# Optimization experiments

Measured on AMD Instinct MI355X. Metric: run time of the kernel, lower is better.

## Reference

```python
import jax, jax.numpy as jnp
import numpy as np

N = 16384


def setup_inputs() -> dict:
    key = jax.random.key(0)
    k1, k2 = jax.random.split(key)
    logits = jax.random.normal(k1, (N,), dtype=jnp.float32)
    targets = jax.random.randint(k2, (N,), 0, 2, dtype=jnp.int64)
    return {"logits": logits, "targets": targets}


def reference(logits, targets):
    # sigmoid scores for every sample
    s = jax.nn.sigmoid(logits)  # [N]
    pos = (targets != 0).astype(s.dtype)  # [N] mask of positives
    neg = (targets == 0).astype(s.dtype)  # [N] mask of negatives
    # all-pairs pos-vs-neg surrogate: (1 - (s_pos - s_neg))^2
    d = 1.0 - (s[:, None] - s[None, :])  # [N, N]
    loss = jnp.sum((pos[:, None] * neg[None, :]) * (d * d))
    n_pos = jnp.sum(pos)
    n_neg = jnp.sum(neg)
    return loss / (n_pos * n_neg)
```

## Files before the change

### kernel.cpp

```cpp
#include <hip/hip_runtime.h>


#define G1 64
#define B1 64

__global__ __launch_bounds__(B1) void auc_partial_kernel(
    const float* __restrict__ logits, const int* __restrict__ targets,
    float* __restrict__ ws, int n) {
  const int gtid = blockIdx.x * B1 + threadIdx.x;
  const int nthreads = G1 * B1;

  float acc[6] = {0.f, 0.f, 0.f, 0.f, 0.f, 0.f};

  const int n4 = n >> 2;
  const float4* l4 = reinterpret_cast<const float4*>(logits);
  const int4*   t4 = reinterpret_cast<const int4*>(targets);

  for (int i = gtid; i < n4; i += nthreads) {
    float4 lv = l4[i];
    int4   tv = t4[i];
    float xs[4] = {lv.x, lv.y, lv.z, lv.w};
    int   ts[4] = {tv.x, tv.y, tv.z, tv.w};
#pragma unroll
    for (int k = 0; k < 4; ++k) {
      float s  = 1.0f / (1.0f + __expf(-xs[k]));
      float s2 = s * s;
      float p  = (ts[k] != 0) ? 1.0f : 0.0f;
      float q  = 1.0f - p;
      acc[0] += p;       acc[1] += q;
      acc[2] += p * s;   acc[3] += q * s;
      acc[4] += p * s2;  acc[5] += q * s2;
    }
  }
  for (int i = (n4 << 2) + gtid; i < n; i += nthreads) {
    float s  = 1.0f / (1.0f + __expf(-logits[i]));
    float s2 = s * s;
    float p  = (targets[i] != 0) ? 1.0f : 0.0f;
    float q  = 1.0f - p;
    acc[0] += p;       acc[1] += q;
    acc[2] += p * s;   acc[3] += q * s;
    acc[4] += p * s2;  acc[5] += q * s2;
  }

#pragma unroll
  for (int j = 0; j < 6; ++j) {
#pragma unroll
    for (int m = 1; m < 64; m <<= 1) {
      acc[j] += __shfl_xor(acc[j], m, 64);
    }
  }

  if (threadIdx.x == 0) {
#pragma unroll
    for (int j = 0; j < 6; ++j) ws[blockIdx.x * 6 + j] = acc[j];
  }
}

__global__ __launch_bounds__(64) void auc_combine_kernel(
    const float* __restrict__ ws, float* __restrict__ out) {
  const int lane = threadIdx.x;

  double t[6];
#pragma unroll
  for (int j = 0; j < 6; ++j) t[j] = (double)ws[lane * 6 + j];

#pragma unroll
  for (int j = 0; j < 6; ++j) {
#pragma unroll
    for (int m = 1; m < 64; m <<= 1) {
      t[j] += __shfl_xor(t[j], m, 64);
    }
  }

  if (lane == 0) {
    double np_ = t[0], nn = t[1], sp = t[2], sn = t[3], sp2 = t[4], sn2 = t[5];
    double loss = np_ * nn
                - 2.0 * nn * sp
                + 2.0 * np_ * sn
                + nn * sp2
                + np_ * sn2
                - 2.0 * sp * sn;
    out[0] = (float)(loss / (np_ * nn));
  }
}

extern "C" void kernel_launch(void* const* d_in, const int* in_sizes, int n_in,
                              void* d_out, int out_size, void* d_ws, size_t ws_size,
                              hipStream_t stream) {
  const float* logits  = (const float*)d_in[0];
  const int*   targets = (const int*)d_in[1];
  float*       out     = (float*)d_out;
  float*       ws      = (float*)d_ws;
  const int n = in_sizes[0];

  auc_partial_kernel<<<dim3(G1), dim3(B1), 0, stream>>>(logits, targets, ws, n);
  auc_combine_kernel<<<dim3(1), dim3(64), 0, stream>>>(ws, out);
}
```

Before: 11.26 us.

## Fuse partial and combine kernels via cooperative grid sync

Merges the two-kernel reduction into a single cooperative kernel. Blocks write their partial sums, synchronize across the grid with cooperative groups, and block 0 then does the final double-precision combine. This removes the second kernel launch and the inter-kernel gap, at the cost of a grid-wide barrier and cooperative-launch overhead, which can be significant on AMD hardware.

```diff
diff --git a/kernel.cpp b/kernel.cpp
--- a/kernel.cpp
+++ b/kernel.cpp
@@ -1,14 +1,18 @@
 #include <hip/hip_runtime.h>
+#include <hip/hip_cooperative_groups.h>
+
+namespace cg = cooperative_groups;
 
 
-#define G1 64
-#define B1 64
+#define GRID 64
+#define BLK  64
 
-__global__ __launch_bounds__(B1) void auc_partial_kernel(
+__global__ __launch_bounds__(BLK) void auc_fused_kernel(
     const float* __restrict__ logits, const int* __restrict__ targets,
-    float* __restrict__ ws, int n) {
-  const int gtid = blockIdx.x * B1 + threadIdx.x;
-  const int nthreads = G1 * B1;
+    float* __restrict__ ws, float* __restrict__ out, int n) {
+  const int tid  = threadIdx.x;
+  const int gtid = blockIdx.x * BLK + tid;
+  const int nthreads = GRID * BLK;
 
   float acc[6] = {0.f, 0.f, 0.f, 0.f, 0.f, 0.f};
 
@@ -50,37 +54,36 @@
     }
   }
 
-  if (threadIdx.x == 0) {
+  if (tid == 0) {
 #pragma unroll
     for (int j = 0; j < 6; ++j) ws[blockIdx.x * 6 + j] = acc[j];
   }
-}
 
-__global__ __launch_bounds__(64) void auc_combine_kernel(
-    const float* __restrict__ ws, float* __restrict__ out) {
-  const int lane = threadIdx.x;
+  cg::this_grid().sync();
 
-  double t[6];
+  if (blockIdx.x == 0) {
+    double t[6];
 #pragma unroll
-  for (int j = 0; j < 6; ++j) t[j] = (double)ws[lane * 6 + j];
+    for (int j = 0; j < 6; ++j) t[j] = (double)ws[tid * 6 + j];
 
 #pragma unroll
-  for (int j = 0; j < 6; ++j) {
+    for (int j = 0; j < 6; ++j) {
 #pragma unroll
-    for (int m = 1; m < 64; m <<= 1) {
-      t[j] += __shfl_xor(t[j], m, 64);
+      for (int m = 1; m < 64; m <<= 1) {
+        t[j] += __shfl_xor(t[j], m, 64);
+      }
     }
-  }
 
-  if (lane == 0) {
-    double np_ = t[0], nn = t[1], sp = t[2], sn = t[3], sp2 = t[4], sn2 = t[5];
-    double loss = np_ * nn
-                - 2.0 * nn * sp
-                + 2.0 * np_ * sn
-                + nn * sp2
-                + np_ * sn2
-                - 2.0 * sp * sn;
-    out[0] = (float)(loss / (np_ * nn));
+    if (tid == 0) {
+      double np_ = t[0], nn = t[1], sp = t[2], sn = t[3], sp2 = t[4], sn2 = t[5];
+      double loss = np_ * nn
+                  - 2.0 * nn * sp
+                  + 2.0 * np_ * sn
+                  + nn * sp2
+                  + np_ * sn2
+                  - 2.0 * sp * sn;
+      out[0] = (float)(loss / (np_ * nn));
+    }
   }
 }
 
@@ -91,8 +94,9 @@
   const int*   targets = (const int*)d_in[1];
   float*       out     = (float*)d_out;
   float*       ws      = (float*)d_ws;
-  const int n = in_sizes[0];
+  int n = in_sizes[0];
 
-  auc_partial_kernel<<<dim3(G1), dim3(B1), 0, stream>>>(logits, targets, ws, n);
-  auc_combine_kernel<<<dim3(1), dim3(64), 0, stream>>>(ws, out);
+  void* args[] = {(void*)&logits, (void*)&targets, (void*)&ws, (void*)&out, (void*)&n};
+  hipLaunchCooperativeKernel((const void*)auc_fused_kernel,
+                             dim3(GRID), dim3(BLK), args, 0, stream);
 }
```

Result: slower. 32.27 us (+186.5%).
